# Kernel optimization log

Measured on AMD Instinct MI355X. Metric: run time of the kernel, lower is better.

Reference implementation:

```python
import jax, jax.numpy as jnp
import numpy as np

B, C, Q, E, H = 8, 1024, 128, 512, 1024


def setup_inputs() -> dict:
    key = jax.random.key(0)
    ks = jax.random.split(key, 8)
    return {
        "context": jax.random.normal(ks[0], (B, C, E), jnp.float32),
        "question": jax.random.normal(ks[1], (B, Q, E), jnp.float32),
        "context_mask": jnp.ones((B, C), jnp.float32),
        "w_question": jax.random.normal(ks[2], (E,), jnp.float32),
        "w_context": jax.random.normal(ks[3], (E,), jnp.float32),
        "w_multiple": jax.random.normal(ks[4], (E,), jnp.float32),
        "W1": jax.random.normal(ks[5], (4 * E, H), jnp.float32) * 0.02,
        "b1": jnp.zeros((H,), jnp.float32),
        "W2": jax.random.normal(ks[6], (H, 4 * E), jnp.float32) * 0.02,
        "b2": jnp.zeros((4 * E,), jnp.float32),
    }


def reference(context, question, context_mask, w_question, w_context, w_multiple, W1, b1, W2, b2):
    # Dropout is identity at eval time.
    # Trilinear similarity: s[b,c,q] = q.w_q + ctx.w_c + sum_e q_e*ctx_e*w_m_e
    q_w = question @ w_question                                  # (B,Q)
    c_w = context @ w_context                                    # (B,C)
    mult = jnp.einsum("bqe,bce->bcq", question * w_multiple, context)  # avoids (B,C,Q,E)
    sim = q_w[:, None, :] + c_w[:, :, None] + mult               # (B,C,Q)

    # Context2Query: softmax over question dim (dim=2)
    c2q = jnp.einsum("bcq,bqe->bce", jax.nn.softmax(sim, axis=2), question)
    # Query2Context: max over question dim, softmax over context dim (dim=1)
    q2c = jnp.einsum("bc,bce->be", jax.nn.softmax(jnp.max(sim, axis=2), axis=1), context)  # (B,E)

    attended = jnp.concatenate(
        [context, c2q, context * c2q, context * q2c[:, None, :]], axis=2
    )  # (B,C,4E)

    # MaskedLinear: linear then zero out masked context positions
    m = context_mask[:, :, None]
    h = (attended @ W1 + b1) * m
    out = jax.nn.relu((h @ W2 + b2) * m)
    return out
```

## Files before the change

kernel.cpp:

```cpp
#include <hip/hip_runtime.h>

typedef __bf16 bf16;
typedef __bf16 bf16x2 __attribute__((ext_vector_type(2)));
typedef __bf16 bf16x4 __attribute__((ext_vector_type(4)));
typedef __bf16 bf16x8 __attribute__((ext_vector_type(8)));
typedef float f32x4 __attribute__((ext_vector_type(4)));

#define AS1 __attribute__((address_space(1)))
#define AS3 __attribute__((address_space(3)))

__device__ __forceinline__ void async_copy16(const void* g, void* l) {
  __builtin_amdgcn_global_load_lds((const AS1 void*)g, (AS3 void*)l, 16, 0, 0);
}

#define BB 8
#define CC 1024
#define QQ 128
#define EE 512
#define HH 1024
#define FOURE 2048

__global__ __launch_bounds__(256) void prep_kernel(
    const float* __restrict__ W1, const float* __restrict__ W2,
    const float* __restrict__ qst, const float* __restrict__ wmul,
    const float* __restrict__ wqv, bf16* __restrict__ W1T,
    bf16* __restrict__ W2T, bf16* __restrict__ qT,
    bf16* __restrict__ qmh, bf16* __restrict__ qml, float* __restrict__ qw,
    float* __restrict__ q2c) {
  __shared__ float tile[32][33];
  __shared__ float r4[4];
  int bx = blockIdx.x;
  int t = threadIdx.x;
  if (bx >= 5120) {
    for (int i = t; i < BB * EE; i += 256) q2c[i] = 0.f;
    return;
  }
  if (bx >= 4608) {
    int i = bx - 4608;
    int half = t >> 7, tr = t & 127;
    int rowg = i * 2 + half;
    const float* qrow = qst + (size_t)rowg * EE;
    float4 qv = *(const float4*)&qrow[tr * 4];
    float4 wm4 = *(const float4*)&wmul[tr * 4];
    float4 wq4 = *(const float4*)&wqv[tr * 4];
    float m[4] = {qv.x * wm4.x, qv.y * wm4.y, qv.z * wm4.z, qv.w * wm4.w};
    bf16x4 h, l;
#pragma unroll
    for (int k = 0; k < 4; ++k) {
      bf16 hh = (bf16)m[k];
      h[k] = hh; l[k] = (bf16)(m[k] - (float)hh);
    }
    *(bf16x4*)&qmh[(size_t)rowg * EE + tr * 4] = h;
    *(bf16x4*)&qml[(size_t)rowg * EE + tr * 4] = l;
    float s = qv.x * wq4.x + qv.y * wq4.y + qv.z * wq4.z + qv.w * wq4.w;
#pragma unroll
    for (int off = 32; off; off >>= 1) s += __shfl_xor(s, off);
    if ((t & 63) == 0) r4[t >> 6] = s;
    __syncthreads();
    if (tr == 0) qw[rowg] = r4[half * 2] + r4[half * 2 + 1];
    return;
  }
  const float* src;
  bf16* dst;
  int R, C, idx;
  if (bx < 2048) {
    src = W1; dst = W1T; R = 2048; C = 1024; idx = bx;
  } else if (bx < 4096) {
    src = W2; dst = W2T; R = 1024; C = 2048; idx = bx - 2048;
  } else {
    int i = bx - 4096;
    int b = i >> 6; idx = i & 63;
    src = qst + (size_t)b * QQ * EE; dst = qT + (size_t)b * EE * QQ;
    R = 128; C = 512;
  }
  int ctiles = C >> 5;
  int by = idx / ctiles, cx = idx % ctiles;
  int tx = t & 31, ty = t >> 5;
#pragma unroll
  for (int rr = 0; rr < 4; ++rr)
    tile[ty + rr * 8][tx] = src[(size_t)(by * 32 + ty + rr * 8) * C + cx * 32 + tx];
  __syncthreads();
#pragma unroll
  for (int rr = 0; rr < 4; ++rr)
    dst[(size_t)(cx * 32 + ty + rr * 8) * R + by * 32 + tx] = (bf16)tile[tx][ty + rr * 8];
}

__global__ __launch_bounds__(256) void fused_att_kernel(
    const float* __restrict__ ctx, const bf16* __restrict__ qmh,
    const bf16* __restrict__ qml, const bf16* __restrict__ qT,
    const float* __restrict__ wc, const float* __restrict__ qw,
    float* __restrict__ smax, bf16* __restrict__ att) {
  __shared__ __align__(16) char U[32768];
  __shared__ float wc_s[EE];
  __shared__ float qw_s[QQ];
  __shared__ float cw_s[16];
  __shared__ bf16 P_lds[16][136];
  int bid = blockIdx.x;
  int t = threadIdx.x;
  int b = bid & 7;
  int m0 = (bid >> 3) * 16;
  bf16* Bh = (bf16*)(U);
  bf16* Bl = (bf16*)(U + 16384);
  float(*sim_s)[132] = (float(*)[132])(U);
  bf16* c2q_lds = (bf16*)(U);
  for (int i = t; i < EE; i += 256) wc_s[i] = wc[i];
  if (t < QQ) qw_s[t] = qw[b * QQ + t];
  int wv = t >> 6, ln = t & 63;
  int rl = ln & 15, kq = ln >> 4;
  const float* Ag = ctx + ((size_t)b * CC + m0) * EE;
  const bf16* Bhg = qmh + (size_t)b * QQ * EE;
  const bf16* Blg = qml + (size_t)b * QQ * EE;
#pragma unroll
  for (int r = 0; r < 2; ++r) {
    int fb = (r * 4 + wv) * 1024 + ln * 16;
    int row = fb >> 6;
    int cq = ((fb >> 4) & 3) ^ ((row >> 1) & 3);
    async_copy16(Bhg + (size_t)row * EE + cq * 8, (char*)Bh + fb);
// ... 129 lines not shown
    bf16* arow_p = att + ((size_t)(b * CC + m0 + row)) * FOURE;
#pragma unroll
    for (int cc = 0; cc < 4; ++cc) {
      int col = cc * 128 + tc * 8;
      bf16x8 q8 = *(const bf16x8*)&c2q_lds[(size_t)row * 520 + col];
      float4 v0 = *(const float4*)&crow[col];
      float4 v1 = *(const float4*)&crow[col + 4];
      float cv[8] = {v0.x, v0.y, v0.z, v0.w, v1.x, v1.y, v1.z, v1.w};
      bf16x8 o0, o2;
#pragma unroll
      for (int k = 0; k < 8; ++k) {
        o0[k] = (bf16)cv[k];
        o2[k] = (bf16)(cv[k] * (float)q8[k]);
      }
      *(bf16x8*)&arow_p[col] = o0;
      *(bf16x8*)&arow_p[EE + col] = q8;
      *(bf16x8*)&arow_p[2 * EE + col] = o2;
    }
  }
}

__global__ __launch_bounds__(256) void q2c_kernel(
    const float* __restrict__ ctx, const float* __restrict__ smax,
    float* __restrict__ q2c) {
  int b = blockIdx.x & 7, ch = blockIdx.x >> 3;
  int t = threadIdx.x;
  __shared__ float red4m[4], red4s[4];
  __shared__ float w_s[32];
  float v[4];
  float mx = -3.4e38f;
#pragma unroll
  for (int i = 0; i < 4; ++i) {
    v[i] = smax[b * CC + i * 256 + t];
    mx = fmaxf(mx, v[i]);
  }
#pragma unroll
  for (int off = 32; off; off >>= 1) mx = fmaxf(mx, __shfl_xor(mx, off));
  if ((t & 63) == 0) red4m[t >> 6] = mx;
  __syncthreads();
  mx = fmaxf(fmaxf(red4m[0], red4m[1]), fmaxf(red4m[2], red4m[3]));
  float sm = 0.f;
#pragma unroll
  for (int i = 0; i < 4; ++i) sm += __expf(v[i] - mx);
#pragma unroll
  for (int off = 32; off; off >>= 1) sm += __shfl_xor(sm, off);
  if ((t & 63) == 0) red4s[t >> 6] = sm;
  __syncthreads();
  float inv = 1.0f / (red4s[0] + red4s[1] + red4s[2] + red4s[3]);
  if (t < 32) w_s[t] = __expf(smax[b * CC + ch * 32 + t] - mx) * inv;
  __syncthreads();
  int e = t * 2;
  const float* cb = ctx + ((size_t)b * CC + ch * 32) * EE;
  float a0 = 0.f, a1 = 0.f;
#pragma unroll 8
  for (int r = 0; r < 32; ++r) {
    float2 vv = *(const float2*)&cb[(size_t)r * EE + e];
    float w = w_s[r];
    a0 += w * vv.x;
    a1 += w * vv.y;
  }
  atomicAdd(&q2c[b * EE + e], a0);
  atomicAdd(&q2c[b * EE + e + 1], a1);
}

__global__ __launch_bounds__(256) void att3_kernel(
    const float* __restrict__ ctx, const float* __restrict__ q2c,
    bf16* __restrict__ att) {
  int b = blockIdx.x & 7;
  int inner = (blockIdx.x >> 3) * 256 + threadIdx.x;
  int row = b * CC + (inner >> 6);
  int e = (inner & 63) * 8;
  float4 v0 = *(const float4*)&ctx[(size_t)row * EE + e];
  float4 v1 = *(const float4*)&ctx[(size_t)row * EE + e + 4];
  float4 g0 = *(const float4*)&q2c[b * EE + e];
  float4 g1 = *(const float4*)&q2c[b * EE + e + 4];
  bf16x8 o;
  o[0] = (bf16)(v0.x * g0.x); o[1] = (bf16)(v0.y * g0.y);
  o[2] = (bf16)(v0.z * g0.z); o[3] = (bf16)(v0.w * g0.w);
  o[4] = (bf16)(v1.x * g1.x); o[5] = (bf16)(v1.y * g1.y);
  o[6] = (bf16)(v1.z * g1.z); o[7] = (bf16)(v1.w * g1.w);
  *(bf16x8*)&att[(size_t)row * FOURE + 3 * EE + e] = o;
}

template <int OUT_BF16, int RELU>
__global__ __launch_bounds__(512, 2) void gemm_bt_p2_kernel(
    const bf16* __restrict__ A, const bf16* __restrict__ Bt,
    const float* __restrict__ bias, const float* __restrict__ mask,
    void* __restrict__ Cout, int M, int N, int K) {
  __shared__ bf16 As[3][256 * 64];
  __shared__ bf16 Bs[3][128 * 64];
  int ntiles = N >> 7;
  int tiles_per_g = 8 * ntiles;
  int g = blockIdx.x / tiles_per_g, sub = blockIdx.x % tiles_per_g;
  int mt = g * 8 + (sub & 7), ntb = sub >> 3;
  int m0 = mt << 8, n0 = ntb << 7;
  int t = threadIdx.x, wv = t >> 6, ln = t & 63;
  int wm = wv >> 1, wn = wv & 1;
  int rl = ln & 15, kq = ln >> 4;
  int NT = K >> 6;

  auto stageA = [&](int buf, int kt, int r) {
    int k0 = kt << 6;
    int fb = r * 8192 + t * 16;
    int row = fb >> 7;
    int q = ((fb >> 4) & 7) ^ (row & 7);
    async_copy16(A + (size_t)(m0 + row) * K + k0 + q * 8, (char*)As[buf] + fb);
  };
  auto stageB = [&](int buf, int kt, int r) {
    int k0 = kt << 6;
    int fb = r * 8192 + t * 16;
    int row = fb >> 7;
    int q = ((fb >> 4) & 7) ^ (row & 7);
    async_copy16(Bt + (size_t)(n0 + row) * K + k0 + q * 8, (char*)Bs[buf] + fb);
  };

#pragma unroll
  for (int r = 0; r < 4; ++r) stageA(0, 0, r);
#pragma unroll
  for (int r = 0; r < 2; ++r) stageB(0, 0, r);
#pragma unroll
  for (int r = 0; r < 4; ++r) stageA(1, 1, r);
#pragma unroll
  for (int r = 0; r < 2; ++r) stageB(1, 1, r);
  asm volatile("s_waitcnt vmcnt(6)" ::: "memory");
  __builtin_amdgcn_s_barrier();

  f32x4 acc[4][4] = {};
  int cur = 0;
  for (int kt = 0; kt < NT; ++kt) {
    const bf16* Ab = As[cur];
    const bf16* Bb = Bs[cur];
    int nxt = cur + 2; if (nxt >= 3) nxt -= 3;
    bool pf = (kt + 2) < NT;
    bf16x8 af0[2][2], bfr[2][4];
#pragma unroll
    for (int ks = 0; ks < 2; ++ks) {
      int c = ks * 4 + kq;
#pragma unroll
      for (int i = 0; i < 2; ++i) {
        int row = wm * 64 + i * 16 + rl;
        af0[ks][i] = *(const bf16x8*)&Ab[row * 64 + ((c ^ (row & 7)) * 8)];
      }
#pragma unroll
      for (int j = 0; j < 4; ++j) {
        int row = wn * 64 + j * 16 + rl;
        bfr[ks][j] = *(const bf16x8*)&Bb[row * 64 + ((c ^ (row & 7)) * 8)];
      }
    }
    if (pf) { stageA(nxt, kt + 2, 0); stageA(nxt, kt + 2, 1); stageA(nxt, kt + 2, 2); }
    __builtin_amdgcn_s_barrier();
    asm volatile("s_waitcnt lgkmcnt(0)" ::: "memory");
    __builtin_amdgcn_sched_barrier(0);
    __builtin_amdgcn_s_setprio(1);
#pragma unroll
    for (int ks = 0; ks < 2; ++ks)
#pragma unroll
      for (int i = 0; i < 2; ++i)
#pragma unroll
        for (int j = 0; j < 4; ++j)
          acc[i][j] = __builtin_amdgcn_mfma_f32_16x16x32_bf16(
              af0[ks][i], bfr[ks][j], acc[i][j], 0, 0, 0);
    __builtin_amdgcn_s_setprio(0);
    __builtin_amdgcn_s_barrier();
    bf16x8 af1[2][2];
#pragma unroll
    for (int ks = 0; ks < 2; ++ks) {
      int c = ks * 4 + kq;
#pragma unroll
      for (int i = 0; i < 2; ++i) {
        int row = wm * 64 + (i + 2) * 16 + rl;
        af1[ks][i] = *(const bf16x8*)&Ab[row * 64 + ((c ^ (row & 7)) * 8)];
      }
    }
    if (pf) { stageA(nxt, kt + 2, 3); stageB(nxt, kt + 2, 0); stageB(nxt, kt + 2, 1); }
    __builtin_amdgcn_s_barrier();
    asm volatile("s_waitcnt lgkmcnt(0)" ::: "memory");
    __builtin_amdgcn_sched_barrier(0);
    __builtin_amdgcn_s_setprio(1);
#pragma unroll
    for (int ks = 0; ks < 2; ++ks)
#pragma unroll
      for (int i = 0; i < 2; ++i)
#pragma unroll
        for (int j = 0; j < 4; ++j)
          acc[i + 2][j] = __builtin_amdgcn_mfma_f32_16x16x32_bf16(
              af1[ks][i], bfr[ks][j], acc[i + 2][j], 0, 0, 0);
    __builtin_amdgcn_s_setprio(0);
    if (kt + 1 < NT) {
      if (pf) asm volatile("s_waitcnt vmcnt(6)" ::: "memory");
      else    asm volatile("s_waitcnt vmcnt(0)" ::: "memory");
      __builtin_amdgcn_s_barrier();
    }
    cur += 1; if (cur >= 3) cur -= 3;
  }

  float bv4[4];
#pragma unroll
  for (int j = 0; j < 4; ++j) bv4[j] = bias[n0 + wn * 64 + j * 16 + rl];
#pragma unroll
  for (int i = 0; i < 4; ++i) {
    int rbase = m0 + wm * 64 + i * 16 + (kq << 2);
#pragma unroll
    for (int r = 0; r < 4; ++r) {
      int row = rbase + r;
      float mk = mask[row];
#pragma unroll
      for (int j = 0; j < 4; ++j) {
        int col = n0 + wn * 64 + j * 16 + rl;
        float v = acc[i][j][r] + bv4[j];
        v *= mk;
        if (RELU) v = fmaxf(v, 0.f);
        if (OUT_BF16)
          ((bf16*)Cout)[(size_t)row * N + col] = (bf16)v;
        else
          ((float*)Cout)[(size_t)row * N + col] = v;
      }
    }
  }
}

template <int OUT_BF16, int RELU>
__global__ __launch_bounds__(512, 2) void gemm_ph8_kernel(
    const bf16* __restrict__ A, const bf16* __restrict__ Bt,
    const float* __restrict__ bias, const float* __restrict__ mask,
    void* __restrict__ Cout, int M, int N, int K) {
  __shared__ bf16 As[2][256 * 64];
  __shared__ bf16 Bs[2][256 * 64];
  int ntn = N >> 8;
  int nblk = (M >> 8) * ntn;
  int cpx = nblk >> 3;
  int swz = (blockIdx.x & 7) * cpx + (blockIdx.x >> 3);
  int mt = swz / ntn, ntb = swz % ntn;
  int m0 = mt << 8, n0 = ntb << 8;
  int t = threadIdx.x, wv = t >> 6, ln = t & 63;
  int wm = wv >> 2, wn = wv & 3;
  int rl = ln & 15, kq = ln >> 4;
  int NT = K >> 6;
  int chunk = t & 7;

  auto stage = [&](int buf, int k1, int arr, int half, int r) {
    int fb = r * 8192 + t * 16;
    int phys = half * 128 + (fb >> 7);
    int q = chunk ^ (phys & 7);
    if (arr == 0) {
      int lg = ((phys >> 6) & 1) * 128 + (phys >> 7) * 64 + (phys & 63);
      async_copy16(A + (size_t)(m0 + lg) * K + k1 + q * 8,
                   (char*)&As[buf][0] + half * 16384 + fb);
    } else {
      int lg = ((phys >> 5) & 3) * 64 + (phys >> 7) * 32 + (phys & 31);
      async_copy16(Bt + (size_t)(n0 + lg) * K + k1 + q * 8,
                   (char*)&Bs[buf][0] + half * 16384 + fb);
    }
  };
  auto ldA = [&](const bf16* Ab, int i, int ks) {
    int pr = (i >> 2) * 128 + wm * 64 + (i & 3) * 16 + rl;
    return *(const bf16x8*)&Ab[pr * 64 + (((ks * 4 + kq) ^ (pr & 7)) * 8)];
  };
  auto ldB = [&](const bf16* Bb, int j, int ks) {
    int pr = (j >> 1) * 128 + wn * 32 + (j & 1) * 16 + rl;
    return *(const bf16x8*)&Bb[pr * 64 + (((ks * 4 + kq) ^ (pr & 7)) * 8)];
  };

  stage(0, 0, 0, 0, 0); stage(0, 0, 0, 0, 1);
  stage(0, 0, 1, 0, 0); stage(0, 0, 1, 0, 1);
  stage(0, 0, 0, 1, 0); stage(0, 0, 0, 1, 1);
  stage(0, 0, 1, 1, 0); stage(0, 0, 1, 1, 1);
  stage(1, 64, 0, 0, 0); stage(1, 64, 0, 0, 1);
  stage(1, 64, 1, 0, 0); stage(1, 64, 1, 0, 1);
  asm volatile("s_waitcnt vmcnt(4)" ::: "memory");
  __builtin_amdgcn_s_barrier();

  f32x4 acc[8][4] = {};
  bf16x8 aX[4][2], bL[2][2], bH[2][2];
  int NI = NT >> 1;
  for (int it = 0; it < NI; ++it) {
    const bf16* A0 = &As[0][0];
    const bf16* B0 = &Bs[0][0];
    const bf16* A1 = &As[1][0];
    const bf16* B1 = &Bs[1][0];
    int t1k = ((it << 1) + 1) << 6;
    int t2k = ((it << 1) + 2) << 6;
    int t3k = ((it << 1) + 3) << 6;
    bool s2 = ((it << 1) + 2) < NT;
    bool s3 = ((it << 1) + 3) < NT;
    bool last = (it == NI - 1);

#pragma unroll
    for (int i = 0; i < 4; ++i) { aX[i][0] = ldA(A0, i, 0); aX[i][1] = ldA(A0, i, 1); }
#pragma unroll
    for (int j = 0; j < 2; ++j) { bL[j][0] = ldB(B0, j, 0); bL[j][1] = ldB(B0, j, 1); }
    stage(1, t1k, 0, 1, 0); stage(1, t1k, 0, 1, 1);
    asm volatile("s_waitcnt lgkmcnt(8)" ::: "memory");
    __builtin_amdgcn_s_barrier();
    asm volatile("s_waitcnt lgkmcnt(0)" ::: "memory");
    __builtin_amdgcn_sched_barrier(0);
    __builtin_amdgcn_s_setprio(1);
#pragma unroll
    for (int ks = 0; ks < 2; ++ks)
#pragma unroll
      for (int i = 0; i < 4; ++i)
#pragma unroll
        for (int j = 0; j < 2; ++j)
          acc[i][j] = __builtin_amdgcn_mfma_f32_16x16x32_bf16(
              aX[i][ks], bL[j][ks], acc[i][j], 0, 0, 0);
    __builtin_amdgcn_s_setprio(0);
    __builtin_amdgcn_s_barrier();
#pragma unroll
    for (int j = 0; j < 2; ++j) { bH[j][0] = ldB(B0, j + 2, 0); bH[j][1] = ldB(B0, j + 2, 1); }
    stage(1, t1k, 1, 1, 0); stage(1, t1k, 1, 1, 1);
    __builtin_amdgcn_s_barrier();
    asm volatile("s_waitcnt lgkmcnt(0)" ::: "memory");
    __builtin_amdgcn_sched_barrier(0);
    __builtin_amdgcn_s_setprio(1);
#pragma unroll
    for (int ks = 0; ks < 2; ++ks)
#pragma unroll
      for (int i = 0; i < 4; ++i)
#pragma unroll
        for (int j = 0; j < 2; ++j)
          acc[i][j + 2] = __builtin_amdgcn_mfma_f32_16x16x32_bf16(
              aX[i][ks], bH[j][ks], acc[i][j + 2], 0, 0, 0);
    __builtin_amdgcn_s_setprio(0);
    __builtin_amdgcn_s_barrier();
#pragma unroll
    for (int i = 0; i < 4; ++i) { aX[i][0] = ldA(A0, i + 4, 0); aX[i][1] = ldA(A0, i + 4, 1); }
    if (s2) { stage(0, t2k, 0, 0, 0); stage(0, t2k, 0, 0, 1); }
    __builtin_amdgcn_s_barrier();
    asm volatile("s_waitcnt lgkmcnt(0)" ::: "memory");
    __builtin_amdgcn_sched_barrier(0);
    __builtin_amdgcn_s_setprio(1);
#pragma unroll
    for (int ks = 0; ks < 2; ++ks)
#pragma unroll
      for (int i = 0; i < 4; ++i)
#pragma unroll
        for (int j = 0; j < 2; ++j)
          acc[i + 4][j] = __builtin_amdgcn_mfma_f32_16x16x32_bf16(
              aX[i][ks], bL[j][ks], acc[i + 4][j], 0, 0, 0);
    __builtin_amdgcn_s_setprio(0);
    __builtin_amdgcn_s_barrier();
    if (s2) { stage(0, t2k, 1, 0, 0); stage(0, t2k, 1, 0, 1); }
    __builtin_amdgcn_s_barrier();
    __builtin_amdgcn_s_setprio(1);
#pragma unroll
    for (int ks = 0; ks < 2; ++ks)
#pragma unroll
      for (int i = 0; i < 4; ++i)
#pragma unroll
        for (int j = 0; j < 2; ++j)
          acc[i + 4][j + 2] = __builtin_amdgcn_mfma_f32_16x16x32_bf16(
              aX[i][ks], bH[j][ks], acc[i + 4][j + 2], 0, 0, 0);
    __builtin_amdgcn_s_setprio(0);
    if (last) asm volatile("s_waitcnt vmcnt(0)" ::: "memory");
    else      asm volatile("s_waitcnt vmcnt(4)" ::: "memory");
    __builtin_amdgcn_s_barrier();
#pragma unroll
    for (int i = 0; i < 4; ++i) { aX[i][0] = ldA(A1, i, 0); aX[i][1] = ldA(A1, i, 1); }
#pragma unroll
    for (int j = 0; j < 2; ++j) { bL[j][0] = ldB(B1, j, 0); bL[j][1] = ldB(B1, j, 1); }
    if (s2) { stage(0, t2k, 0, 1, 0); stage(0, t2k, 0, 1, 1); }
    asm volatile("s_waitcnt lgkmcnt(8)" ::: "memory");
    __builtin_amdgcn_s_barrier();
    asm volatile("s_waitcnt lgkmcnt(0)" ::: "memory");
    __builtin_amdgcn_sched_barrier(0);
    __builtin_amdgcn_s_setprio(1);
#pragma unroll
    for (int ks = 0; ks < 2; ++ks)
#pragma unroll
      for (int i = 0; i < 4; ++i)
#pragma unroll
        for (int j = 0; j < 2; ++j)
          acc[i][j] = __builtin_amdgcn_mfma_f32_16x16x32_bf16(
              aX[i][ks], bL[j][ks], acc[i][j], 0, 0, 0);
    __builtin_amdgcn_s_setprio(0);
    __builtin_amdgcn_s_barrier();
#pragma unroll
    for (int j = 0; j < 2; ++j) { bH[j][0] = ldB(B1, j + 2, 0); bH[j][1] = ldB(B1, j + 2, 1); }
    if (s2) { stage(0, t2k, 1, 1, 0); stage(0, t2k, 1, 1, 1); }
    __builtin_amdgcn_s_barrier();
    asm volatile("s_waitcnt lgkmcnt(0)" ::: "memory");
    __builtin_amdgcn_sched_barrier(0);
    __builtin_amdgcn_s_setprio(1);
#pragma unroll
    for (int ks = 0; ks < 2; ++ks)
#pragma unroll
      for (int i = 0; i < 4; ++i)
#pragma unroll
        for (int j = 0; j < 2; ++j)
          acc[i][j + 2] = __builtin_amdgcn_mfma_f32_16x16x32_bf16(
              aX[i][ks], bH[j][ks], acc[i][j + 2], 0, 0, 0);
    __builtin_amdgcn_s_setprio(0);
    __builtin_amdgcn_s_barrier();
#pragma unroll
    for (int i = 0; i < 4; ++i) { aX[i][0] = ldA(A1, i + 4, 0); aX[i][1] = ldA(A1, i + 4, 1); }
    if (s3) { stage(1, t3k, 0, 0, 0); stage(1, t3k, 0, 0, 1); }
    __builtin_amdgcn_s_barrier();
    asm volatile("s_waitcnt lgkmcnt(0)" ::: "memory");
    __builtin_amdgcn_sched_barrier(0);
    __builtin_amdgcn_s_setprio(1);
#pragma unroll
    for (int ks = 0; ks < 2; ++ks)
#pragma unroll
      for (int i = 0; i < 4; ++i)
#pragma unroll
        for (int j = 0; j < 2; ++j)
          acc[i + 4][j] = __builtin_amdgcn_mfma_f32_16x16x32_bf16(
              aX[i][ks], bL[j][ks], acc[i + 4][j], 0, 0, 0);
    __builtin_amdgcn_s_setprio(0);
    __builtin_amdgcn_s_barrier();
    if (s3) { stage(1, t3k, 1, 0, 0); stage(1, t3k, 1, 0, 1); }
    __builtin_amdgcn_s_barrier();
    __builtin_amdgcn_s_setprio(1);
#pragma unroll
    for (int ks = 0; ks < 2; ++ks)
#pragma unroll
      for (int i = 0; i < 4; ++i)
#pragma unroll
        for (int j = 0; j < 2; ++j)
          acc[i + 4][j + 2] = __builtin_amdgcn_mfma_f32_16x16x32_bf16(
              aX[i][ks], bH[j][ks], acc[i + 4][j + 2], 0, 0, 0);
    __builtin_amdgcn_s_setprio(0);
    if (!last) {
      asm volatile("s_waitcnt vmcnt(4)" ::: "memory");
      __builtin_amdgcn_s_barrier();
    }
  }

  float bv4[4];
#pragma unroll
  for (int j = 0; j < 4; ++j) bv4[j] = bias[n0 + wn * 64 + j * 16 + rl];
#pragma unroll
  for (int i = 0; i < 8; ++i) {
    int rbase = m0 + wm * 128 + i * 16 + (kq << 2);
#pragma unroll
    for (int r = 0; r < 4; ++r) {
      int row = rbase + r;
      float mk = mask[row];
#pragma unroll
      for (int j = 0; j < 4; ++j) {
        int col = n0 + wn * 64 + j * 16 + rl;
        float v = acc[i][j][r] + bv4[j];
        v *= mk;
        if (RELU) v = fmaxf(v, 0.f);
        if (OUT_BF16)
          ((bf16*)Cout)[(size_t)row * N + col] = (bf16)v;
        else
          ((float*)Cout)[(size_t)row * N + col] = v;
      }
    }
  }
}

extern "C" void kernel_launch(void* const* d_in, const int* in_sizes, int n_in,
                              void* d_out, int out_size, void* d_ws, size_t ws_size,
                              hipStream_t stream) {
  const float* ctx = (const float*)d_in[0];
  const float* qst = (const float*)d_in[1];
  const float* mask = (const float*)d_in[2];
  const float* wqv = (const float*)d_in[3];
  const float* wcv = (const float*)d_in[4];
  const float* wmul = (const float*)d_in[5];
  const float* W1 = (const float*)d_in[6];
  const float* b1 = (const float*)d_in[7];
  const float* W2 = (const float*)d_in[8];
  const float* b2 = (const float*)d_in[9];
  float* out = (float*)d_out;
  char* ws = (char*)d_ws;

  bf16* att = (bf16*)(ws);
  bf16* hbuf = (bf16*)(ws + 33554432);
  bf16* W1T = (bf16*)(ws + 50331648);
  bf16* W2T = (bf16*)(ws + 54525952);
  bf16* qT = (bf16*)(ws + 58720256);
  bf16* qmh = (bf16*)(ws + 59768832);
  bf16* qml = (bf16*)(ws + 60817408);
  float* smax = (float*)(ws + 61865984);
  float* q2c = (float*)(ws + 61898752);
  float* qw = (float*)(ws + 61915136);

  prep_kernel<<<5121, 256, 0, stream>>>(W1, W2, qst, wmul, wqv,
                                        W1T, W2T, qT, qmh, qml, qw, q2c);
  fused_att_kernel<<<512, 256, 0, stream>>>(ctx, qmh, qml, qT, wcv,
                                            qw, smax, att);
  q2c_kernel<<<256, 256, 0, stream>>>(ctx, smax, q2c);
  att3_kernel<<<2048, 256, 0, stream>>>(ctx, q2c, att);
  gemm_bt_p2_kernel<1, 0><<<256, 512, 0, stream>>>(
      att, W1T, b1, mask, hbuf, 8192, 1024, 2048);
  gemm_ph8_kernel<0, 1><<<256, 512, 0, stream>>>(
      hbuf, W2T, b2, mask, out, 8192, 2048, 1024);
}
```

Measured before the change: 216.3 us.

## Fuse both MLP GEMMs into one persistent kernel with per-row-tile flags

Merges the W1 GEMM and the W2 GEMM into a single kernel launch. Each of the 256 blocks first computes one 256x128 tile of the hidden activations, then signals an atomic counter for its 256-row band. It spins until all 8 blocks of that band have finished, and only then computes a 256x256 tile of the output. This removes one kernel launch and the full-device boundary between the GEMMs, and may keep hbuf hot in L2. It relies on all 256 blocks being co-resident, since otherwise the spin-wait can deadlock. It also uses one shared LDS buffer sized for the larger stage, which may reduce occupancy.

```diff
diff --git a/kernel.cpp b/kernel.cpp
--- a/kernel.cpp
+++ b/kernel.cpp
@@ -26,13 +26,14 @@
     const float* __restrict__ wqv, bf16* __restrict__ W1T,
     bf16* __restrict__ W2T, bf16* __restrict__ qT,
     bf16* __restrict__ qmh, bf16* __restrict__ qml, float* __restrict__ qw,
-    float* __restrict__ q2c) {
+    float* __restrict__ q2c, unsigned* __restrict__ flags) {
   __shared__ float tile[32][33];
   __shared__ float r4[4];
   int bx = blockIdx.x;
   int t = threadIdx.x;
   if (bx >= 5120) {
     for (int i = t; i < BB * EE; i += 256) q2c[i] = 0.f;
+    if (t < 32) flags[t] = 0u;
     return;
   }
   if (bx >= 4608) {
@@ -328,370 +329,367 @@
   *(bf16x8*)&att[(size_t)row * FOURE + 3 * EE + e] = o;
 }
 
-template <int OUT_BF16, int RELU>
-__global__ __launch_bounds__(512, 2) void gemm_bt_p2_kernel(
-    const bf16* __restrict__ A, const bf16* __restrict__ Bt,
-    const float* __restrict__ bias, const float* __restrict__ mask,
-    void* __restrict__ Cout, int M, int N, int K) {
-  __shared__ bf16 As[3][256 * 64];
-  __shared__ bf16 Bs[3][128 * 64];
-  int ntiles = N >> 7;
-  int tiles_per_g = 8 * ntiles;
-  int g = blockIdx.x / tiles_per_g, sub = blockIdx.x % tiles_per_g;
-  int mt = g * 8 + (sub & 7), ntb = sub >> 3;
-  int m0 = mt << 8, n0 = ntb << 7;
+__global__ __launch_bounds__(512, 2) void gemm_fused_kernel(
+    const bf16* __restrict__ attA, const bf16* __restrict__ W1T,
+    const float* __restrict__ b1, bf16* __restrict__ hbuf,
+    const bf16* __restrict__ W2T, const float* __restrict__ b2,
+    const float* __restrict__ mask, float* __restrict__ out,
+    unsigned* __restrict__ flags) {
+  __shared__ __align__(16) char LDSU[147456];
+  int bid = blockIdx.x;
   int t = threadIdx.x, wv = t >> 6, ln = t & 63;
-  int wm = wv >> 1, wn = wv & 1;
   int rl = ln & 15, kq = ln >> 4;
-  int NT = K >> 6;
-
-  auto stageA = [&](int buf, int kt, int r) {
-    int k0 = kt << 6;
-    int fb = r * 8192 + t * 16;
-    int row = fb >> 7;
-    int q = ((fb >> 4) & 7) ^ (row & 7);
-    async_copy16(A + (size_t)(m0 + row) * K + k0 + q * 8, (char*)As[buf] + fb);
-  };
-  auto stageB = [&](int buf, int kt, int r) {
-    int k0 = kt << 6;
-    int fb = r * 8192 + t * 16;
-    int row = fb >> 7;
-    int q = ((fb >> 4) & 7) ^ (row & 7);
-    async_copy16(Bt + (size_t)(n0 + row) * K + k0 + q * 8, (char*)Bs[buf] + fb);
-  };
-
-#pragma unroll
-  for (int r = 0; r < 4; ++r) stageA(0, 0, r);
-#pragma unroll
-  for (int r = 0; r < 2; ++r) stageB(0, 0, r);
-#pragma unroll
-  for (int r = 0; r < 4; ++r) stageA(1, 1, r);
-#pragma unroll
-  for (int r = 0; r < 2; ++r) stageB(1, 1, r);
-  asm volatile("s_waitcnt vmcnt(6)" ::: "memory");
-  __builtin_amdgcn_s_barrier();
-
-  f32x4 acc[4][4] = {};
-  int cur = 0;
-  for (int kt = 0; kt < NT; ++kt) {
-    const bf16* Ab = As[cur];
-    const bf16* Bb = Bs[cur];
-    int nxt = cur + 2; if (nxt >= 3) nxt -= 3;
-    bool pf = (kt + 2) < NT;
-    bf16x8 af0[2][2], bfr[2][4];
-#pragma unroll
-    for (int ks = 0; ks < 2; ++ks) {
-      int c = ks * 4 + kq;
-#pragma unroll
-      for (int i = 0; i < 2; ++i) {
-        int row = wm * 64 + i * 16 + rl;
-        af0[ks][i] = *(const bf16x8*)&Ab[row * 64 + ((c ^ (row & 7)) * 8)];
-      }
-#pragma unroll
-      for (int j = 0; j < 4; ++j) {
-        int row = wn * 64 + j * 16 + rl;
-        bfr[ks][j] = *(const bf16x8*)&Bb[row * 64 + ((c ^ (row & 7)) * 8)];
-      }
-    }
-    if (pf) { stageA(nxt, kt + 2, 0); stageA(nxt, kt + 2, 1); stageA(nxt, kt + 2, 2); }
+  int mt = bid >> 3;
+  int m0 = mt << 8;
+
+  {
+    const int K = 2048, N = 1024;
+    int n0 = (bid & 7) << 7;
+    int wm = wv >> 1, wn = wv & 1;
+    int NT = K >> 6;
+    auto As = [&](int buf) { return (bf16*)(LDSU + buf * 32768); };
+    auto Bs = [&](int buf) { return (bf16*)(LDSU + 98304 + buf * 16384); };
+    auto stageA = [&](int buf, int kt, int r) {
+      int k0 = kt << 6;
+      int fb = r * 8192 + t * 16;
+      int row = fb >> 7;
+      int q = ((fb >> 4) & 7) ^ (row & 7);
+      async_copy16(attA + (size_t)(m0 + row) * K + k0 + q * 8,
+                   (char*)As(buf) + fb);
+    };
+    auto stageB = [&](int buf, int kt, int r) {
+      int k0 = kt << 6;
+      int fb = r * 8192 + t * 16;
+      int row = fb >> 7;
+      int q = ((fb >> 4) & 7) ^ (row & 7);
+      async_copy16(W1T + (size_t)(n0 + row) * K + k0 + q * 8,
+                   (char*)Bs(buf) + fb);
+    };
+#pragma unroll
+    for (int r = 0; r < 4; ++r) stageA(0, 0, r);
+#pragma unroll
+    for (int r = 0; r < 2; ++r) stageB(0, 0, r);
+#pragma unroll
+    for (int r = 0; r < 4; ++r) stageA(1, 1, r);
+#pragma unroll
+    for (int r = 0; r < 2; ++r) stageB(1, 1, r);
+    asm volatile("s_waitcnt vmcnt(6)" ::: "memory");
     __builtin_amdgcn_s_barrier();
-    asm volatile("s_waitcnt lgkmcnt(0)" ::: "memory");
-    __builtin_amdgcn_sched_barrier(0);
-    __builtin_amdgcn_s_setprio(1);
-#pragma unroll
-    for (int ks = 0; ks < 2; ++ks)
-#pragma unroll
-      for (int i = 0; i < 2; ++i)
-#pragma unroll
-        for (int j = 0; j < 4; ++j)
-          acc[i][j] = __builtin_amdgcn_mfma_f32_16x16x32_bf16(
-              af0[ks][i], bfr[ks][j], acc[i][j], 0, 0, 0);
-    __builtin_amdgcn_s_setprio(0);
+
+    f32x4 acc[4][4] = {};
+    int cur = 0;
+    for (int kt = 0; kt < NT; ++kt) {
+      const bf16* Ab = As(cur);
+      const bf16* Bb = Bs(cur);
+      int nxt = cur + 2; if (nxt >= 3) nxt -= 3;
+      bool pf = (kt + 2) < NT;
+      bf16x8 af0[2][2], bfr[2][4];
+#pragma unroll
+      for (int ks = 0; ks < 2; ++ks) {
+        int c = ks * 4 + kq;
+#pragma unroll
+        for (int i = 0; i < 2; ++i) {
+          int row = wm * 64 + i * 16 + rl;
+          af0[ks][i] = *(const bf16x8*)&Ab[row * 64 + ((c ^ (row & 7)) * 8)];
+        }
+#pragma unroll
+        for (int j = 0; j < 4; ++j) {
+          int row = wn * 64 + j * 16 + rl;
+          bfr[ks][j] = *(const bf16x8*)&Bb[row * 64 + ((c ^ (row & 7)) * 8)];
+        }
+      }
+      if (pf) { stageA(nxt, kt + 2, 0); stageA(nxt, kt + 2, 1); stageA(nxt, kt + 2, 2); }
+      __builtin_amdgcn_s_barrier();
+      asm volatile("s_waitcnt lgkmcnt(0)" ::: "memory");
+      __builtin_amdgcn_sched_barrier(0);
+      __builtin_amdgcn_s_setprio(1);
+#pragma unroll
+      for (int ks = 0; ks < 2; ++ks)
+#pragma unroll
+        for (int i = 0; i < 2; ++i)
+#pragma unroll
+          for (int j = 0; j < 4; ++j)
+            acc[i][j] = __builtin_amdgcn_mfma_f32_16x16x32_bf16(
+                af0[ks][i], bfr[ks][j], acc[i][j], 0, 0, 0);
+      __builtin_amdgcn_s_setprio(0);
+      __builtin_amdgcn_s_barrier();
+      bf16x8 af1[2][2];
+#pragma unroll
+      for (int ks = 0; ks < 2; ++ks) {
+        int c = ks * 4 + kq;
+#pragma unroll
+        for (int i = 0; i < 2; ++i) {
+          int row = wm * 64 + (i + 2) * 16 + rl;
+          af1[ks][i] = *(const bf16x8*)&Ab[row * 64 + ((c ^ (row & 7)) * 8)];
+        }
+      }
+      if (pf) { stageA(nxt, kt + 2, 3); stageB(nxt, kt + 2, 0); stageB(nxt, kt + 2, 1); }
+      __builtin_amdgcn_s_barrier();
+      asm volatile("s_waitcnt lgkmcnt(0)" ::: "memory");
+      __builtin_amdgcn_sched_barrier(0);
+      __builtin_amdgcn_s_setprio(1);
+#pragma unroll
+      for (int ks = 0; ks < 2; ++ks)
+#pragma unroll
+        for (int i = 0; i < 2; ++i)
+#pragma unroll
+          for (int j = 0; j < 4; ++j)
+            acc[i + 2][j] = __builtin_amdgcn_mfma_f32_16x16x32_bf16(
+                af1[ks][i], bfr[ks][j], acc[i + 2][j], 0, 0, 0);
+      __builtin_amdgcn_s_setprio(0);
+      if (kt + 1 < NT) {
+        if (pf) asm volatile("s_waitcnt vmcnt(6)" ::: "memory");
+        else    asm volatile("s_waitcnt vmcnt(0)" ::: "memory");
+        __builtin_amdgcn_s_barrier();
+      }
+      cur += 1; if (cur >= 3) cur -= 3;
+    }
+    float bv4[4];
+#pragma unroll
+    for (int j = 0; j < 4; ++j) bv4[j] = b1[n0 + wn * 64 + j * 16 + rl];
+#pragma unroll
+    for (int i = 0; i < 4; ++i) {
+      int rbase = m0 + wm * 64 + i * 16 + (kq << 2);
+#pragma unroll
+      for (int r = 0; r < 4; ++r) {
+        int row = rbase + r;
+        float mk = mask[row];
+#pragma unroll
+        for (int j = 0; j < 4; ++j) {
+          int col = n0 + wn * 64 + j * 16 + rl;
+          float v = acc[i][j][r] + bv4[j];
+          v *= mk;
+          hbuf[(size_t)row * N + col] = (bf16)v;
+        }
+      }
+    }
+  }
+
+  __threadfence();
+  __syncthreads();
+  if (t == 0) {
+    __hip_atomic_fetch_add(&flags[mt], 1u, __ATOMIC_RELEASE,
+                           __HIP_MEMORY_SCOPE_AGENT);
+    while (__hip_atomic_load(&flags[mt], __ATOMIC_ACQUIRE,
+                             __HIP_MEMORY_SCOPE_AGENT) < 8u)
+      __builtin_amdgcn_s_sleep(2);
+  }
+  __syncthreads();
+
+  {
+    const int K = 1024, N = 2048;
+    int n0 = (bid & 7) << 8;
+    int wm = wv >> 2, wn = wv & 3;
+    int NT = K >> 6;
+    int chunk = t & 7;
+    auto As2 = [&](int buf) { return (bf16*)(LDSU + buf * 32768); };
+    auto Bs2 = [&](int buf) { return (bf16*)(LDSU + 65536 + buf * 32768); };
+    auto stage = [&](int buf, int k1, int arr, int half, int r) {
+      int fb = r * 8192 + t * 16;
+      int phys = half * 128 + (fb >> 7);
+      int q = chunk ^ (phys & 7);
+      if (arr == 0) {
+        int lg = ((phys >> 6) & 1) * 128 + (phys >> 7) * 64 + (phys & 63);
+        async_copy16(hbuf + (size_t)(m0 + lg) * K + k1 + q * 8,
+                     (char*)As2(buf) + half * 16384 + fb);
+      } else {
+        int lg = ((phys >> 5) & 3) * 64 + (phys >> 7) * 32 + (phys & 31);
+        async_copy16(W2T + (size_t)(n0 + lg) * K + k1 + q * 8,
+                     (char*)Bs2(buf) + half * 16384 + fb);
+      }
+    };
+    auto ldA = [&](const bf16* Ab, int i, int ks) {
+      int pr = (i >> 2) * 128 + wm * 64 + (i & 3) * 16 + rl;
+      return *(const bf16x8*)&Ab[pr * 64 + (((ks * 4 + kq) ^ (pr & 7)) * 8)];
+    };
+    auto ldB = [&](const bf16* Bb, int j, int ks) {
+      int pr = (j >> 1) * 128 + wn * 32 + (j & 1) * 16 + rl;
+      return *(const bf16x8*)&Bb[pr * 64 + (((ks * 4 + kq) ^ (pr & 7)) * 8)];
+    };
+
+    stage(0, 0, 0, 0, 0); stage(0, 0, 0, 0, 1);
+    stage(0, 0, 1, 0, 0); stage(0, 0, 1, 0, 1);
+    stage(0, 0, 0, 1, 0); stage(0, 0, 0, 1, 1);
+    stage(0, 0, 1, 1, 0); stage(0, 0, 1, 1, 1);
+    stage(1, 64, 0, 0, 0); stage(1, 64, 0, 0, 1);
+    stage(1, 64, 1, 0, 0); stage(1, 64, 1, 0, 1);
+    asm volatile("s_waitcnt vmcnt(4)" ::: "memory");
     __builtin_amdgcn_s_barrier();
-    bf16x8 af1[2][2];
-#pragma unroll
-    for (int ks = 0; ks < 2; ++ks) {
-      int c = ks * 4 + kq;
-#pragma unroll
-      for (int i = 0; i < 2; ++i) {
-        int row = wm * 64 + (i + 2) * 16 + rl;
-        af1[ks][i] = *(const bf16x8*)&Ab[row * 64 + ((c ^ (row & 7)) * 8)];
-      }
-    }
-    if (pf) { stageA(nxt, kt + 2, 3); stageB(nxt, kt + 2, 0); stageB(nxt, kt + 2, 1); }
-    __builtin_amdgcn_s_barrier();
-    asm volatile("s_waitcnt lgkmcnt(0)" ::: "memory");
-    __builtin_amdgcn_sched_barrier(0);
-    __builtin_amdgcn_s_setprio(1);
-#pragma unroll
-    for (int ks = 0; ks < 2; ++ks)
-#pragma unroll
-      for (int i = 0; i < 2; ++i)
-#pragma unroll
-        for (int j = 0; j < 4; ++j)
-          acc[i + 2][j] = __builtin_amdgcn_mfma_f32_16x16x32_bf16(
-              af1[ks][i], bfr[ks][j], acc[i + 2][j], 0, 0, 0);
-    __builtin_amdgcn_s_setprio(0);
-    if (kt + 1 < NT) {
-      if (pf) asm volatile("s_waitcnt vmcnt(6)" ::: "memory");
-      else    asm volatile("s_waitcnt vmcnt(0)" ::: "memory");
-      __builtin_amdgcn_s_barrier();
-    }
-    cur += 1; if (cur >= 3) cur -= 3;
-  }
-
-  float bv4[4];
-#pragma unroll
-  for (int j = 0; j < 4; ++j) bv4[j] = bias[n0 + wn * 64 + j * 16 + rl];
-#pragma unroll
-  for (int i = 0; i < 4; ++i) {
-    int rbase = m0 + wm * 64 + i * 16 + (kq << 2);
-#pragma unroll
-    for (int r = 0; r < 4; ++r) {
-      int row = rbase + r;
-      float mk = mask[row];
-#pragma unroll
-      for (int j = 0; j < 4; ++j) {
-        int col = n0 + wn * 64 + j * 16 + rl;
-        float v = acc[i][j][r] + bv4[j];
-        v *= mk;
-        if (RELU) v = fmaxf(v, 0.f);
-        if (OUT_BF16)
-          ((bf16*)Cout)[(size_t)row * N + col] = (bf16)v;
-        else
-          ((float*)Cout)[(size_t)row * N + col] = v;
-      }
-    }
-  }
-}
-
-template <int OUT_BF16, int RELU>
-__global__ __launch_bounds__(512, 2) void gemm_ph8_kernel(
-    const bf16* __restrict__ A, const bf16* __restrict__ Bt,
-    const float* __restrict__ bias, const float* __restrict__ mask,
-    void* __restrict__ Cout, int M, int N, int K) {
-  __shared__ bf16 As[2][256 * 64];
-  __shared__ bf16 Bs[2][256 * 64];
-  int ntn = N >> 8;
-  int nblk = (M >> 8) * ntn;
-  int cpx = nblk >> 3;
-  int swz = (blockIdx.x & 7) * cpx + (blockIdx.x >> 3);
-  int mt = swz / ntn, ntb = swz % ntn;
-  int m0 = mt << 8, n0 = ntb << 8;
-  int t = threadIdx.x, wv = t >> 6, ln = t & 63;
-  int wm = wv >> 2, wn = wv & 3;
-  int rl = ln & 15, kq = ln >> 4;
-  int NT = K >> 6;
-  int chunk = t & 7;
-
-  auto stage = [&](int buf, int k1, int arr, int half, int r) {
-    int fb = r * 8192 + t * 16;
-    int phys = half * 128 + (fb >> 7);
-    int q = chunk ^ (phys & 7);
-    if (arr == 0) {
-      int lg = ((phys >> 6) & 1) * 128 + (phys >> 7) * 64 + (phys & 63);
-      async_copy16(A + (size_t)(m0 + lg) * K + k1 + q * 8,
-                   (char*)&As[buf][0] + half * 16384 + fb);
-    } else {
-      int lg = ((phys >> 5) & 3) * 64 + (phys >> 7) * 32 + (phys & 31);
-      async_copy16(Bt + (size_t)(n0 + lg) * K + k1 + q * 8,
-                   (char*)&Bs[buf][0] + half * 16384 + fb);
-    }
-  };
-  auto ldA = [&](const bf16* Ab, int i, int ks) {
-    int pr = (i >> 2) * 128 + wm * 64 + (i & 3) * 16 + rl;
-    return *(const bf16x8*)&Ab[pr * 64 + (((ks * 4 + kq) ^ (pr & 7)) * 8)];
-  };
-  auto ldB = [&](const bf16* Bb, int j, int ks) {
-    int pr = (j >> 1) * 128 + wn * 32 + (j & 1) * 16 + rl;
-    return *(const bf16x8*)&Bb[pr * 64 + (((ks * 4 + kq) ^ (pr & 7)) * 8)];
-  };
-
-  stage(0, 0, 0, 0, 0); stage(0, 0, 0, 0, 1);
-  stage(0, 0, 1, 0, 0); stage(0, 0, 1, 0, 1);
-  stage(0, 0, 0, 1, 0); stage(0, 0, 0, 1, 1);
-  stage(0, 0, 1, 1, 0); stage(0, 0, 1, 1, 1);
-  stage(1, 64, 0, 0, 0); stage(1, 64, 0, 0, 1);
-  stage(1, 64, 1, 0, 0); stage(1, 64, 1, 0, 1);
-  asm volatile("s_waitcnt vmcnt(4)" ::: "memory");
-  __builtin_amdgcn_s_barrier();
-
-  f32x4 acc[8][4] = {};
-  bf16x8 aX[4][2], bL[2][2], bH[2][2];
-  int NI = NT >> 1;
-  for (int it = 0; it < NI; ++it) {
-    const bf16* A0 = &As[0][0];
-    const bf16* B0 = &Bs[0][0];
-    const bf16* A1 = &As[1][0];
-    const bf16* B1 = &Bs[1][0];
-    int t1k = ((it << 1) + 1) << 6;
-    int t2k = ((it << 1) + 2) << 6;
-    int t3k = ((it << 1) + 3) << 6;
-    bool s2 = ((it << 1) + 2) < NT;
-    bool s3 = ((it << 1) + 3) < NT;
-    bool last = (it == NI - 1);
-
-#pragma unroll
-    for (int i = 0; i < 4; ++i) { aX[i][0] = ldA(A0, i, 0); aX[i][1] = ldA(A0, i, 1); }
-#pragma unroll
-    for (int j = 0; j < 2; ++j) { bL[j][0] = ldB(B0, j, 0); bL[j][1] = ldB(B0, j, 1); }
-    stage(1, t1k, 0, 1, 0); stage(1, t1k, 0, 1, 1);
-    asm volatile("s_waitcnt lgkmcnt(8)" ::: "memory");
-    __builtin_amdgcn_s_barrier();
-    asm volatile("s_waitcnt lgkmcnt(0)" ::: "memory");
-    __builtin_amdgcn_sched_barrier(0);
-    __builtin_amdgcn_s_setprio(1);
-#pragma unroll
-    for (int ks = 0; ks < 2; ++ks)
-#pragma unroll
-      for (int i = 0; i < 4; ++i)
-#pragma unroll
-        for (int j = 0; j < 2; ++j)
-          acc[i][j] = __builtin_amdgcn_mfma_f32_16x16x32_bf16(
-              aX[i][ks], bL[j][ks], acc[i][j], 0, 0, 0);
-    __builtin_amdgcn_s_setprio(0);
-    __builtin_amdgcn_s_barrier();
-#pragma unroll
-    for (int j = 0; j < 2; ++j) { bH[j][0] = ldB(B0, j + 2, 0); bH[j][1] = ldB(B0, j + 2, 1); }
-    stage(1, t1k, 1, 1, 0); stage(1, t1k, 1, 1, 1);
-    __builtin_amdgcn_s_barrier();
-    asm volatile("s_waitcnt lgkmcnt(0)" ::: "memory");
-    __builtin_amdgcn_sched_barrier(0);
-    __builtin_amdgcn_s_setprio(1);
-#pragma unroll
-    for (int ks = 0; ks < 2; ++ks)
-#pragma unroll
-      for (int i = 0; i < 4; ++i)
-#pragma unroll
-        for (int j = 0; j < 2; ++j)
-          acc[i][j + 2] = __builtin_amdgcn_mfma_f32_16x16x32_bf16(
-              aX[i][ks], bH[j][ks], acc[i][j + 2], 0, 0, 0);
-    __builtin_amdgcn_s_setprio(0);
-    __builtin_amdgcn_s_barrier();
-#pragma unroll
-    for (int i = 0; i < 4; ++i) { aX[i][0] = ldA(A0, i + 4, 0); aX[i][1] = ldA(A0, i + 4, 1); }
-    if (s2) { stage(0, t2k, 0, 0, 0); stage(0, t2k, 0, 0, 1); }
-    __builtin_amdgcn_s_barrier();
-    asm volatile("s_waitcnt lgkmcnt(0)" ::: "memory");
-    __builtin_amdgcn_sched_barrier(0);
-    __builtin_amdgcn_s_setprio(1);
-#pragma unroll
-    for (int ks = 0; ks < 2; ++ks)
-#pragma unroll
-      for (int i = 0; i < 4; ++i)
-#pragma unroll
-        for (int j = 0; j < 2; ++j)
-          acc[i + 4][j] = __builtin_amdgcn_mfma_f32_16x16x32_bf16(
-              aX[i][ks], bL[j][ks], acc[i + 4][j], 0, 0, 0);
-    __builtin_amdgcn_s_setprio(0);
-    __builtin_amdgcn_s_barrier();
-    if (s2) { stage(0, t2k, 1, 0, 0); stage(0, t2k, 1, 0, 1); }
-    __builtin_amdgcn_s_barrier();
-    __builtin_amdgcn_s_setprio(1);
-#pragma unroll
-    for (int ks = 0; ks < 2; ++ks)
-#pragma unroll
-      for (int i = 0; i < 4; ++i)
-#pragma unroll
-        for (int j = 0; j < 2; ++j)
-          acc[i + 4][j + 2] = __builtin_amdgcn_mfma_f32_16x16x32_bf16(
-              aX[i][ks], bH[j][ks], acc[i + 4][j + 2], 0, 0, 0);
-    __builtin_amdgcn_s_setprio(0);
-    if (last) asm volatile("s_waitcnt vmcnt(0)" ::: "memory");
-    else      asm volatile("s_waitcnt vmcnt(4)" ::: "memory");
-    __builtin_amdgcn_s_barrier();
-#pragma unroll
-    for (int i = 0; i < 4; ++i) { aX[i][0] = ldA(A1, i, 0); aX[i][1] = ldA(A1, i, 1); }
-#pragma unroll
-    for (int j = 0; j < 2; ++j) { bL[j][0] = ldB(B1, j, 0); bL[j][1] = ldB(B1, j, 1); }
-    if (s2) { stage(0, t2k, 0, 1, 0); stage(0, t2k, 0, 1, 1); }
-    asm volatile("s_waitcnt lgkmcnt(8)" ::: "memory");
-    __builtin_amdgcn_s_barrier();
-    asm volatile("s_waitcnt lgkmcnt(0)" ::: "memory");
-    __builtin_amdgcn_sched_barrier(0);
-    __builtin_amdgcn_s_setprio(1);
-#pragma unroll
-    for (int ks = 0; ks < 2; ++ks)
-#pragma unroll
-      for (int i = 0; i < 4; ++i)
-#pragma unroll
-        for (int j = 0; j < 2; ++j)
-          acc[i][j] = __builtin_amdgcn_mfma_f32_16x16x32_bf16(
-              aX[i][ks], bL[j][ks], acc[i][j], 0, 0, 0);
-    __builtin_amdgcn_s_setprio(0);
-    __builtin_amdgcn_s_barrier();
-#pragma unroll
-    for (int j = 0; j < 2; ++j) { bH[j][0] = ldB(B1, j + 2, 0); bH[j][1] = ldB(B1, j + 2, 1); }
-    if (s2) { stage(0, t2k, 1, 1, 0); stage(0, t2k, 1, 1, 1); }
-    __builtin_amdgcn_s_barrier();
-    asm volatile("s_waitcnt lgkmcnt(0)" ::: "memory");
-    __builtin_amdgcn_sched_barrier(0);
-    __builtin_amdgcn_s_setprio(1);
-#pragma unroll
-    for (int ks = 0; ks < 2; ++ks)
-#pragma unroll
-      for (int i = 0; i < 4; ++i)
-#pragma unroll
-        for (int j = 0; j < 2; ++j)
-          acc[i][j + 2] = __builtin_amdgcn_mfma_f32_16x16x32_bf16(
-              aX[i][ks], bH[j][ks], acc[i][j + 2], 0, 0, 0);
-    __builtin_amdgcn_s_setprio(0);
-    __builtin_amdgcn_s_barrier();
-#pragma unroll
-    for (int i = 0; i < 4; ++i) { aX[i][0] = ldA(A1, i + 4, 0); aX[i][1] = ldA(A1, i + 4, 1); }
-    if (s3) { stage(1, t3k, 0, 0, 0); stage(1, t3k, 0, 0, 1); }
-    __builtin_amdgcn_s_barrier();
-    asm volatile("s_waitcnt lgkmcnt(0)" ::: "memory");
-    __builtin_amdgcn_sched_barrier(0);
-    __builtin_amdgcn_s_setprio(1);
-#pragma unroll
-    for (int ks = 0; ks < 2; ++ks)
-#pragma unroll
-      for (int i = 0; i < 4; ++i)
-#pragma unroll
-        for (int j = 0; j < 2; ++j)
-          acc[i + 4][j] = __builtin_amdgcn_mfma_f32_16x16x32_bf16(
-              aX[i][ks], bL[j][ks], acc[i + 4][j], 0, 0, 0);
-    __builtin_amdgcn_s_setprio(0);
-    __builtin_amdgcn_s_barrier();
-    if (s3) { stage(1, t3k, 1, 0, 0); stage(1, t3k, 1, 0, 1); }
-    __builtin_amdgcn_s_barrier();
-    __builtin_amdgcn_s_setprio(1);
-#pragma unroll
-    for (int ks = 0; ks < 2; ++ks)
-#pragma unroll
-      for (int i = 0; i < 4; ++i)
-#pragma unroll
-        for (int j = 0; j < 2; ++j)
-          acc[i + 4][j + 2] = __builtin_amdgcn_mfma_f32_16x16x32_bf16(
-              aX[i][ks], bH[j][ks], acc[i + 4][j + 2], 0, 0, 0);
-    __builtin_amdgcn_s_setprio(0);
-    if (!last) {
-      asm volatile("s_waitcnt vmcnt(4)" ::: "memory");
-      __builtin_amdgcn_s_barrier();
-    }
-  }
-
-  float bv4[4];
-#pragma unroll
-  for (int j = 0; j < 4; ++j) bv4[j] = bias[n0 + wn * 64 + j * 16 + rl];
-#pragma unroll
-  for (int i = 0; i < 8; ++i) {
-    int rbase = m0 + wm * 128 + i * 16 + (kq << 2);
-#pragma unroll
-    for (int r = 0; r < 4; ++r) {
-      int row = rbase + r;
-      float mk = mask[row];
-#pragma unroll
-      for (int j = 0; j < 4; ++j) {
-        int col = n0 + wn * 64 + j * 16 + rl;
-        float v = acc[i][j][r] + bv4[j];
-        v *= mk;
-        if (RELU) v = fmaxf(v, 0.f);
-        if (OUT_BF16)
-          ((bf16*)Cout)[(size_t)row * N + col] = (bf16)v;
-        else
-          ((float*)Cout)[(size_t)row * N + col] = v;
+
+    f32x4 acc[8][4] = {};
+    bf16x8 aX[4][2], bL[2][2], bH[2][2];
+    int NI = NT >> 1;
+    for (int it = 0; it < NI; ++it) {
+      const bf16* A0 = As2(0);
+      const bf16* B0 = Bs2(0);
+      const bf16* A1 = As2(1);
+      const bf16* B1 = Bs2(1);
+      int t1k = ((it << 1) + 1) << 6;
+      int t2k = ((it << 1) + 2) << 6;
+      int t3k = ((it << 1) + 3) << 6;
+      bool s2 = ((it << 1) + 2) < NT;
+      bool s3 = ((it << 1) + 3) < NT;
+      bool last = (it == NI - 1);
+
+#pragma unroll
+      for (int i = 0; i < 4; ++i) { aX[i][0] = ldA(A0, i, 0); aX[i][1] = ldA(A0, i, 1); }
+#pragma unroll
+      for (int j = 0; j < 2; ++j) { bL[j][0] = ldB(B0, j, 0); bL[j][1] = ldB(B0, j, 1); }
+      stage(1, t1k, 0, 1, 0); stage(1, t1k, 0, 1, 1);
+      asm volatile("s_waitcnt lgkmcnt(8)" ::: "memory");
+      __builtin_amdgcn_s_barrier();
+      asm volatile("s_waitcnt lgkmcnt(0)" ::: "memory");
+      __builtin_amdgcn_sched_barrier(0);
+      __builtin_amdgcn_s_setprio(1);
+#pragma unroll
+      for (int ks = 0; ks < 2; ++ks)
+#pragma unroll
+        for (int i = 0; i < 4; ++i)
+#pragma unroll
+          for (int j = 0; j < 2; ++j)
+            acc[i][j] = __builtin_amdgcn_mfma_f32_16x16x32_bf16(
+                aX[i][ks], bL[j][ks], acc[i][j], 0, 0, 0);
+      __builtin_amdgcn_s_setprio(0);
+      __builtin_amdgcn_s_barrier();
+#pragma unroll
+      for (int j = 0; j < 2; ++j) { bH[j][0] = ldB(B0, j + 2, 0); bH[j][1] = ldB(B0, j + 2, 1); }
+      stage(1, t1k, 1, 1, 0); stage(1, t1k, 1, 1, 1);
+      __builtin_amdgcn_s_barrier();
+      asm volatile("s_waitcnt lgkmcnt(0)" ::: "memory");
+      __builtin_amdgcn_sched_barrier(0);
+      __builtin_amdgcn_s_setprio(1);
+#pragma unroll
+      for (int ks = 0; ks < 2; ++ks)
+#pragma unroll
+        for (int i = 0; i < 4; ++i)
+#pragma unroll
+          for (int j = 0; j < 2; ++j)
+            acc[i][j + 2] = __builtin_amdgcn_mfma_f32_16x16x32_bf16(
+                aX[i][ks], bH[j][ks], acc[i][j + 2], 0, 0, 0);
+      __builtin_amdgcn_s_setprio(0);
+      __builtin_amdgcn_s_barrier();
+#pragma unroll
+      for (int i = 0; i < 4; ++i) { aX[i][0] = ldA(A0, i + 4, 0); aX[i][1] = ldA(A0, i + 4, 1); }
+      if (s2) { stage(0, t2k, 0, 0, 0); stage(0, t2k, 0, 0, 1); }
+      __builtin_amdgcn_s_barrier();
+      asm volatile("s_waitcnt lgkmcnt(0)" ::: "memory");
+      __builtin_amdgcn_sched_barrier(0);
+      __builtin_amdgcn_s_setprio(1);
+#pragma unroll
+      for (int ks = 0; ks < 2; ++ks)
+#pragma unroll
+        for (int i = 0; i < 4; ++i)
+#pragma unroll
+          for (int j = 0; j < 2; ++j)
+            acc[i + 4][j] = __builtin_amdgcn_mfma_f32_16x16x32_bf16(
+                aX[i][ks], bL[j][ks], acc[i + 4][j], 0, 0, 0);
+      __builtin_amdgcn_s_setprio(0);
+      __builtin_amdgcn_s_barrier();
+      if (s2) { stage(0, t2k, 1, 0, 0); stage(0, t2k, 1, 0, 1); }
+      __builtin_amdgcn_s_barrier();
+      __builtin_amdgcn_s_setprio(1);
+#pragma unroll
+      for (int ks = 0; ks < 2; ++ks)
+#pragma unroll
+        for (int i = 0; i < 4; ++i)
+#pragma unroll
+          for (int j = 0; j < 2; ++j)
+            acc[i + 4][j + 2] = __builtin_amdgcn_mfma_f32_16x16x32_bf16(
+                aX[i][ks], bH[j][ks], acc[i + 4][j + 2], 0, 0, 0);
+      __builtin_amdgcn_s_setprio(0);
+      if (last) asm volatile("s_waitcnt vmcnt(0)" ::: "memory");
+      else      asm volatile("s_waitcnt vmcnt(4)" ::: "memory");
+      __builtin_amdgcn_s_barrier();
+#pragma unroll
+      for (int i = 0; i < 4; ++i) { aX[i][0] = ldA(A1, i, 0); aX[i][1] = ldA(A1, i, 1); }
+#pragma unroll
+      for (int j = 0; j < 2; ++j) { bL[j][0] = ldB(B1, j, 0); bL[j][1] = ldB(B1, j, 1); }
+      if (s2) { stage(0, t2k, 0, 1, 0); stage(0, t2k, 0, 1, 1); }
+      asm volatile("s_waitcnt lgkmcnt(8)" ::: "memory");
+      __builtin_amdgcn_s_barrier();
+      asm volatile("s_waitcnt lgkmcnt(0)" ::: "memory");
+      __builtin_amdgcn_sched_barrier(0);
+      __builtin_amdgcn_s_setprio(1);
+#pragma unroll
+      for (int ks = 0; ks < 2; ++ks)
+#pragma unroll
+        for (int i = 0; i < 4; ++i)
+#pragma unroll
+          for (int j = 0; j < 2; ++j)
+            acc[i][j] = __builtin_amdgcn_mfma_f32_16x16x32_bf16(
+                aX[i][ks], bL[j][ks], acc[i][j], 0, 0, 0);
+      __builtin_amdgcn_s_setprio(0);
+      __builtin_amdgcn_s_barrier();
+#pragma unroll
+      for (int j = 0; j < 2; ++j) { bH[j][0] = ldB(B1, j + 2, 0); bH[j][1] = ldB(B1, j + 2, 1); }
+      if (s2) { stage(0, t2k, 1, 1, 0); stage(0, t2k, 1, 1, 1); }
+      __builtin_amdgcn_s_barrier();
+      asm volatile("s_waitcnt lgkmcnt(0)" ::: "memory");
+      __builtin_amdgcn_sched_barrier(0);
+      __builtin_amdgcn_s_setprio(1);
+#pragma unroll
+      for (int ks = 0; ks < 2; ++ks)
+#pragma unroll
+        for (int i = 0; i < 4; ++i)
+#pragma unroll
+          for (int j = 0; j < 2; ++j)
+            acc[i][j + 2] = __builtin_amdgcn_mfma_f32_16x16x32_bf16(
+                aX[i][ks], bH[j][ks], acc[i][j + 2], 0, 0, 0);
+      __builtin_amdgcn_s_setprio(0);
+      __builtin_amdgcn_s_barrier();
+#pragma unroll
+      for (int i = 0; i < 4; ++i) { aX[i][0] = ldA(A1, i + 4, 0); aX[i][1] = ldA(A1, i + 4, 1); }
+      if (s3) { stage(1, t3k, 0, 0, 0); stage(1, t3k, 0, 0, 1); }
+      __builtin_amdgcn_s_barrier();
+      asm volatile("s_waitcnt lgkmcnt(0)" ::: "memory");
+      __builtin_amdgcn_sched_barrier(0);
+      __builtin_amdgcn_s_setprio(1);
+#pragma unroll
+      for (int ks = 0; ks < 2; ++ks)
+#pragma unroll
+        for (int i = 0; i < 4; ++i)
+#pragma unroll
+          for (int j = 0; j < 2; ++j)
+            acc[i + 4][j] = __builtin_amdgcn_mfma_f32_16x16x32_bf16(
+                aX[i][ks], bL[j][ks], acc[i + 4][j], 0, 0, 0);
+      __builtin_amdgcn_s_setprio(0);
+      __builtin_amdgcn_s_barrier();
+      if (s3) { stage(1, t3k, 1, 0, 0); stage(1, t3k, 1, 0, 1); }
+      __builtin_amdgcn_s_barrier();
+      __builtin_amdgcn_s_setprio(1);
+#pragma unroll
+      for (int ks = 0; ks < 2; ++ks)
+#pragma unroll
+        for (int i = 0; i < 4; ++i)
+#pragma unroll
+          for (int j = 0; j < 2; ++j)
+            acc[i + 4][j + 2] = __builtin_amdgcn_mfma_f32_16x16x32_bf16(
+                aX[i][ks], bH[j][ks], acc[i + 4][j + 2], 0, 0, 0);
+      __builtin_amdgcn_s_setprio(0);
+      if (!last) {
+        asm volatile("s_waitcnt vmcnt(4)" ::: "memory");
+        __builtin_amdgcn_s_barrier();
+      }
+    }
+
+    float bv4[4];
+#pragma unroll
+    for (int j = 0; j < 4; ++j) bv4[j] = b2[n0 + wn * 64 + j * 16 + rl];
+#pragma unroll
+    for (int i = 0; i < 8; ++i) {
+      int rbase = m0 + wm * 128 + i * 16 + (kq << 2);
+#pragma unroll
+      for (int r = 0; r < 4; ++r) {
+        int row = rbase + r;
+        float mk = mask[row];
+#pragma unroll
+        for (int j = 0; j < 4; ++j) {
+          int col = n0 + wn * 64 + j * 16 + rl;
+          float v = acc[i][j][r] + bv4[j];
+          v *= mk;
+          v = fmaxf(v, 0.f);
+          out[(size_t)row * N + col] = v;
+        }
       }
     }
   }
@@ -723,15 +721,14 @@
   float* smax = (float*)(ws + 61865984);
   float* q2c = (float*)(ws + 61898752);
   float* qw = (float*)(ws + 61915136);
+  unsigned* flags = (unsigned*)(ws + 61919232);
 
   prep_kernel<<<5121, 256, 0, stream>>>(W1, W2, qst, wmul, wqv,
-                                        W1T, W2T, qT, qmh, qml, qw, q2c);
+                                        W1T, W2T, qT, qmh, qml, qw, q2c, flags);
   fused_att_kernel<<<512, 256, 0, stream>>>(ctx, qmh, qml, qT, wcv,
                                             qw, smax, att);
   q2c_kernel<<<256, 256, 0, stream>>>(ctx, smax, q2c);
   att3_kernel<<<2048, 256, 0, stream>>>(ctx, q2c, att);
-  gemm_bt_p2_kernel<1, 0><<<256, 512, 0, stream>>>(
-      att, W1T, b1, mask, hbuf, 8192, 1024, 2048);
-  gemm_ph8_kernel<0, 1><<<256, 512, 0, stream>>>(
-      hbuf, W2T, b2, mask, out, 8192, 2048, 1024);
+  gemm_fused_kernel<<<256, 512, 0, stream>>>(att, W1T, b1, hbuf,
+                                             W2T, b2, mask, out, flags);
 }
```

Result: slower. 308.0 us (+42.4%).
